# Kernel tuning notes

Hardware: AMD Instinct MI355X
Metric: run time of the kernel (lower is better)

## Reference

```python
import jax, jax.numpy as jnp
import numpy as np

NEG = -9e8

def _leaky(x):
    return jax.nn.leaky_relu(x, 0.01)

def _gru(x, h, wih, whh, bih, bhh):
    # torch.nn.GRUCell math
    gi = x @ wih.T + bih
    gh = h @ whh.T + bhh
    ir, iz, inn = jnp.split(gi, 3, axis=-1)
    hr, hz, hn = jnp.split(gh, 3, axis=-1)
    r = jax.nn.sigmoid(ir + hr)
    z = jax.nn.sigmoid(iz + hz)
    n = jnp.tanh(inn + r * hn)
    return (1.0 - z) * n + z * h

def _gather(feat, idx):
    # feat [B,S,F], idx [B,S,K] -> [B,S,K,F]; -1 wraps to last row, masked later (same as torch)
    return jax.vmap(lambda f, i: f[i])(feat, idx)

def setup_inputs() -> dict:
    key = jax.random.key(0)
    ks = jax.random.split(key, 32)
    B, S, K, F_in, E, R = 32, 512, 21, 26, 256, 3
    amino_list = jax.random.uniform(ks[0], (B, S, F_in), dtype=jnp.float32)
    idx = jax.random.randint(ks[1], (B, S, K), 0, S, dtype=jnp.int32)
    pad = jax.random.uniform(ks[2], (B, S, K)) < 0.3
    amino_degree_list = jnp.where(pad, jnp.int32(-1), idx)
    # variable sequence lengths for mask
    lens = jax.random.randint(ks[3], (B,), S // 2, S + 1)
    amino_mask = (jnp.arange(S)[None, :] < lens[:, None]).astype(jnp.float32)
    s = 0.05
    d = dict(
        amino_list=amino_list,
        amino_degree_list=amino_degree_list,
        amino_mask=amino_mask,
        emb_W=jax.random.normal(ks[4], (E, F_in)) * s,
        emb_b=jax.random.normal(ks[5], (E,)) * s,
        neigh_W=jax.random.normal(ks[6], (E, F_in)) * s,
        neigh_b=jax.random.normal(ks[7], (E,)) * s,
        align_W=jax.random.normal(ks[8], (R, 1, 2 * E)) * s,
        align_b=jax.random.normal(ks[9], (R, 1)) * s,
        attend_W=jax.random.normal(ks[10], (R, E, E)) * s,
        attend_b=jax.random.normal(ks[11], (R, E)) * s,
        gru_wih=jax.random.normal(ks[12], (R, 3 * E, E)) * s,
        gru_whh=jax.random.normal(ks[13], (R, 3 * E, E)) * s,
        gru_bih=jax.random.normal(ks[14], (R, 3 * E)) * s,
        gru_bhh=jax.random.normal(ks[15], (R, 3 * E)) * s,
        seq_align_W=jax.random.normal(ks[16], (1, 2 * E)) * s,
        seq_align_b=jax.random.normal(ks[17], (1,)) * s,
        seq_attend_W=jax.random.normal(ks[18], (E, E)) * s,
        seq_attend_b=jax.random.normal(ks[19], (E,)) * s,
        sgru_wih=jax.random.normal(ks[20], (3 * E, E)) * s,
        sgru_whh=jax.random.normal(ks[21], (3 * E, E)) * s,
        sgru_bih=jax.random.normal(ks[22], (3 * E,)) * s,
        sgru_bhh=jax.random.normal(ks[23], (3 * E,)) * s,
    )
    return d

RADIUS = 3
T_STEPS = 2

def reference(amino_list, amino_degree_list, amino_mask,
              emb_W, emb_b, neigh_W, neigh_b,
              align_W, align_b, attend_W, attend_b,
              gru_wih, gru_whh, gru_bih, gru_bhh,
              seq_align_W, seq_align_b, seq_attend_W, seq_attend_b,
              sgru_wih, sgru_whh, sgru_bih, sgru_bhh):
    B, S, _ = amino_list.shape
    E = emb_W.shape[0]
    K = amino_degree_list.shape[-1]

    mask3 = amino_mask[:, :, None]                       # [B,S,1]
    amino_feature = _leaky(amino_list @ emb_W.T + emb_b)  # [B,S,E]

    attend_mask = (amino_degree_list != -1).astype(jnp.float32)[..., None]   # [B,S,K,1]
    softmax_mask = jnp.where(amino_degree_list == -1, NEG, 0.0)[..., None]   # [B,S,K,1]

    # first radius step: neighbors from raw one-hot features via neighbor_fc
    neighbor = _gather(amino_list, amino_degree_list)                 # [B,S,K,F_in]
    neighbor_feature = _leaky(neighbor @ neigh_W.T + neigh_b)         # [B,S,K,E]

    h = amino_feature.reshape(B * S, E)
    activated = None
    for d in range(RADIUS):
        if d == 0:
            nbr = neighbor_feature
            cur = amino_feature
        else:
            nbr = _gather(activated, amino_degree_list)               # [B,S,K,E]
            cur = activated
        cur_exp = jnp.broadcast_to(cur[:, :, None, :], (B, S, K, E))
        feat_align = jnp.concatenate([cur_exp, nbr], axis=-1)         # [B,S,K,2E]
        score = _leaky(feat_align @ align_W[d].T + align_b[d]) + softmax_mask
        attw = jax.nn.softmax(score, axis=-2) * attend_mask           # [B,S,K,1]
        nbr_t = nbr @ attend_W[d].T + attend_b[d]                     # [B,S,K,E]
        context = jax.nn.elu(jnp.sum(attw * nbr_t, axis=-2))          # [B,S,E]
        h = _gru(context.reshape(B * S, E), h, gru_wih[d], gru_whh[d], gru_bih[d], gru_bhh[d])
        activated = jax.nn.relu(h.reshape(B, S, E))

    seq_feature = jnp.sum(activated * mask3, axis=-2)                 # [B,E]
    act_mol = jax.nn.relu(seq_feature)
    seq_softmax_mask = jnp.where(mask3 == 0.0, NEG, 0.0)              # [B,S,1]

    act_seq = act_mol
    for _ in range(T_STEPS):
        mol_exp = jnp.broadcast_to(act_mol[:, None, :], (B, S, E))
        sa = jnp.concatenate([mol_exp, activated], axis=-1)           # [B,S,2E]
        score = _leaky(sa @ seq_align_W.T + seq_align_b) + seq_softmax_mask
        w = jax.nn.softmax(score, axis=-2) * mask3                    # [B,S,1]
        feat_t = activated @ seq_attend_W.T + seq_attend_b            # [B,S,E]
        seq_context = jax.nn.elu(jnp.sum(w * feat_t, axis=-2))        # [B,E]
        seq_feature = _gru(seq_context, seq_feature, sgru_wih, sgru_whh, sgru_bih, sgru_bhh)
        act_seq = jax.nn.relu(seq_feature)
    return act_seq
```

## Files before the change

kernel.cpp:

```cpp
#include <hip/hip_runtime.h>
#include <hip/hip_bf16.h>
#include <math.h>


#define NEGC (-9.0e8f)

typedef __attribute__((ext_vector_type(8))) short bf16x8;
typedef __attribute__((ext_vector_type(4))) float f32x4;

__device__ __forceinline__ ushort f2bf(float x) {
    union { float f; unsigned u; } v; v.f = x;
    unsigned r = v.u + 0x7FFF + ((v.u >> 16) & 1);
    return (ushort)(r >> 16);
}
__device__ __forceinline__ float bf2f(ushort u) {
    union { unsigned u; float f; } v; v.u = ((unsigned)u) << 16;
    return v.f;
}
__device__ __forceinline__ float sigm_fast(float x) {
    return 1.f / (1.f + __expf(-x));
}
__device__ __forceinline__ float tanh_fast(float x) {
    return 1.f - 2.f / (__expf(2.f * x) + 1.f);
}
__device__ __forceinline__ float elu_fast(float x) {
    return x > 0.f ? x : (__expf(x) - 1.f);
}

typedef const __attribute__((address_space(1))) void gvoid_t;
typedef __attribute__((address_space(3))) void lvoid_t;

__global__ __launch_bounds__(256) void cvt4_kernel(
    const float* __restrict__ s0, ushort* __restrict__ d0, int n0,
    const float* __restrict__ s1, ushort* __restrict__ d1, int n1,
    const float* __restrict__ s2, ushort* __restrict__ d2, int n2,
    const float* __restrict__ s3, ushort* __restrict__ d3, int n3)
{
    int i = blockIdx.x * 256 + threadIdx.x;
    const float* s; ushort* dst; int l;
    if (i < n0) { s = s0; dst = d0; l = i; }
    else if (i < n0 + n1) { s = s1; dst = d1; l = i - n0; }
    else if (i < n0 + n1 + n2) { s = s2; dst = d2; l = i - n0 - n1; }
    else if (i < n0 + n1 + n2 + n3) { s = s3; dst = d3; l = i - n0 - n1 - n2; }
    else return;
    float4 v = *reinterpret_cast<const float4*>(s + (size_t)l * 4);
    ushort4 o; o.x = f2bf(v.x); o.y = f2bf(v.y); o.z = f2bf(v.z); o.w = f2bf(v.w);
    *reinterpret_cast<ushort4*>(dst + (size_t)l * 4) = o;
}

__global__ __launch_bounds__(256) void gemm_dual_kernel(
    const ushort* __restrict__ A0, const ushort* __restrict__ W0,
    const float* __restrict__ b0, ushort* __restrict__ C0, int n0t,
    const ushort* __restrict__ A1, const ushort* __restrict__ W1,
    const float* __restrict__ b1, ushort* __restrict__ C1, int n1t,
    int K,
    const float* __restrict__ dw1, const float* __restrict__ dw2,
    float* __restrict__ dout1, float* __restrict__ dout2)
{
    __shared__ __align__(16) short As[128 * 32];
    __shared__ __align__(16) short Bs[128 * 32];
    int nwg = gridDim.x;
    int q = nwg >> 3;
    int flat = blockIdx.x;
    int sw = (flat & 7) * q + (flat >> 3);
    int tot = n0t + n1t;
    int bmi = sw / tot, bni = sw - bmi * tot;
    const ushort* A; const ushort* W; const float* bias; ushort* C; int N, bn;
    if (bni < n0t) { A = A0; W = W0; bias = b0; C = C0; N = n0t << 7; bn = bni << 7; }
    else { A = A1; W = W1; bias = b1; C = C1; N = n1t << 7; bn = (bni - n0t) << 7; }
    int bm = bmi << 7;

    int tid = threadIdx.x;
    int lane = tid & 63;
    int w = tid >> 6;
    int wr = w >> 1, wc = w & 1;
    bool dots = (dout1 != nullptr) && (bni == 0);

    f32x4 acc[4][4];
#pragma unroll
    for (int m = 0; m < 4; ++m)
#pragma unroll
        for (int n = 0; n < 4; ++n) acc[m][n] = (f32x4){0.f, 0.f, 0.f, 0.f};
    float p1 = 0.f, p2 = 0.f;

    for (int k0 = 0; k0 < K; k0 += 32) {
#pragma unroll
        for (int i = 0; i < 2; ++i) {
            int e = w * 1024 + i * 512 + lane * 8;
            int r = e >> 5, c = e & 31;
            const ushort* ga = A + (size_t)(bm + r) * K + (k0 + c);
            const ushort* gw = W + (size_t)(bn + r) * K + (k0 + c);
            __builtin_amdgcn_global_load_lds((gvoid_t*)ga, (lvoid_t*)&As[w * 1024 + i * 512], 16, 0, 0);
            __builtin_amdgcn_global_load_lds((gvoid_t*)gw, (lvoid_t*)&Bs[w * 1024 + i * 512], 16, 0, 0);
        }
        __syncthreads();
        bf16x8 af[4], bw[4];
        int ra = wr * 64 + (lane & 15);
        int rb = wc * 64 + (lane & 15);
        int kc = (lane >> 4) * 8;
#pragma unroll
        for (int m = 0; m < 4; ++m)
            af[m] = *reinterpret_cast<const bf16x8*>(&As[(ra + m * 16) * 32 + kc]);
#pragma unroll
        for (int n = 0; n < 4; ++n)
            bw[n] = *reinterpret_cast<const bf16x8*>(&Bs[(rb + n * 16) * 32 + kc]);
#pragma unroll
        for (int m = 0; m < 4; ++m)
#pragma unroll
            for (int n = 0; n < 4; ++n)
                acc[m][n] = __builtin_amdgcn_mfma_f32_16x16x32_bf16(af[m], bw[n], acc[m][n], 0, 0, 0);
        if (dots) {
            int drow = tid >> 1, kh = (tid & 1) << 4;
            const short* ar = &As[drow * 32 + kh];
#pragma unroll
            for (int c = 0; c < 16; ++c) {
                float av = bf2f((ushort)ar[c]);
                p1 = fmaf(av, dw1[k0 + kh + c], p1);
                if (dw2) p2 = fmaf(av, dw2[k0 + kh + c], p2);
            }
        }
        __syncthreads();
    }

    if (dots) {
        p1 += __shfl_xor(p1, 1);
        if (dw2) p2 += __shfl_xor(p2, 1);
        if ((tid & 1) == 0) {
            dout1[bm + (tid >> 1)] = p1;
            if (dw2) dout2[bm + (tid >> 1)] = p2;
        }
    }

    int cr0 = bm + wr * 64 + ((lane >> 4) * 4);
    int cc0 = bn + wc * 64 + (lane & 15);
#pragma unroll
    for (int n = 0; n < 4; ++n) {
        int col = cc0 + n * 16;
        float bv = bias[col];
#pragma unroll
        for (int m = 0; m < 4; ++m) {
            int row0 = cr0 + m * 16;
#pragma unroll
            for (int j = 0; j < 4; ++j) {
                float v = acc[m][n][j] + bv;
                C[(size_t)(row0 + j) * N + col] = f2bf(v);
            }
        }
    }
}

__global__ __launch_bounds__(256) void gru_fused_kernel(
    const ushort* __restrict__ ctx, const ushort* __restrict__ wih,
    const float* __restrict__ bih, const ushort* __restrict__ whh,
    const float* __restrict__ bhh,
    const ushort* __restrict__ h_in, ushort* __restrict__ h_out,
    ushort* __restrict__ act_bf)
{
    __shared__ __align__(16) short lds[16384];
    int flat = blockIdx.x;
    int sw = (flat & 7) * 128 + (flat >> 3);
    int bmi = sw >> 2, ct = sw & 3;
    int bm = bmi << 6;
    int tid = threadIdx.x;
    int lane = tid & 63;
    int w = tid >> 6;
    int wr = w >> 1, wc = w & 1;

    f32x4 acc[6][2][2];
#pragma unroll
    for (int qq = 0; qq < 6; ++qq)
#pragma unroll
        for (int m = 0; m < 2; ++m)
#pragma unroll
            for (int n = 0; n < 2; ++n) acc[qq][m][n] = (f32x4){0.f, 0.f, 0.f, 0.f};

    int srow = tid >> 2, scol = (tid & 3) << 3;
    int ldst = (tid & 0xC0) * 8;
    for (int k0 = 0; k0 < 256; k0 += 32) {
        {
            const ushort* s0 = ctx  + (size_t)(bm + srow) * 256 + k0 + scol;
            const ushort* s1 = h_in + (size_t)(bm + srow) * 256 + k0 + scol;
            __builtin_amdgcn_global_load_lds((gvoid_t*)s0, (lvoid_t*)&lds[ldst], 16, 0, 0);
            __builtin_amdgcn_global_load_lds((gvoid_t*)s1, (lvoid_t*)&lds[2048 + ldst], 16, 0, 0);
#pragma unroll
            for (int qq = 0; qq < 6; ++qq) {
                const ushort* wb = (qq < 3) ? wih : whh;
                int slice = (qq < 3) ? qq : qq - 3;
                const ushort* sv = wb + (size_t)(slice * 256 + ct * 64 + srow) * 256 + k0 + scol;
                __builtin_amdgcn_global_load_lds((gvoid_t*)sv,
                    (lvoid_t*)&lds[(2 + qq) * 2048 + ldst], 16, 0, 0);
            }
        }
        __syncthreads();
        int rl = lane & 15;
        int kc = (lane >> 4) * 8;
        bf16x8 a_c[2], a_h[2];
#pragma unroll
        for (int m = 0; m < 2; ++m) {
            a_c[m] = *reinterpret_cast<const bf16x8*>(&lds[(wr * 32 + m * 16 + rl) * 32 + kc]);
            a_h[m] = *reinterpret_cast<const bf16x8*>(&lds[2048 + (wr * 32 + m * 16 + rl) * 32 + kc]);
        }
#pragma unroll
        for (int qq = 0; qq < 6; ++qq) {
            bf16x8 bw[2];
#pragma unroll
            for (int n = 0; n < 2; ++n)
                bw[n] = *reinterpret_cast<const bf16x8*>(
                    &lds[(2 + qq) * 2048 + (wc * 32 + n * 16 + rl) * 32 + kc]);
#pragma unroll
            for (int m = 0; m < 2; ++m)
#pragma unroll
                for (int n = 0; n < 2; ++n)
                    acc[qq][m][n] = __builtin_amdgcn_mfma_f32_16x16x32_bf16(
                        (qq < 3) ? a_c[m] : a_h[m], bw[n], acc[qq][m][n], 0, 0, 0);
        }
        __syncthreads();
    }

#pragma unroll
    for (int n = 0; n < 2; ++n) {
        int col = ct * 64 + wc * 32 + n * 16 + (lane & 15);
        float bir = bih[col], biz = bih[256 + col], bin = bih[512 + col];
        float bhr = bhh[col], bhz = bhh[256 + col], bhn = bhh[512 + col];
#pragma unroll
        for (int m = 0; m < 2; ++m) {
            int row0 = bm + wr * 32 + m * 16 + ((lane >> 4) * 4);
#pragma unroll
            for (int j = 0; j < 4; ++j) {
                size_t idx = (size_t)(row0 + j) * 256 + col;
                float r = sigm_fast(acc[0][m][n][j] + bir + acc[3][m][n][j] + bhr);
                float z = sigm_fast(acc[1][m][n][j] + biz + acc[4][m][n][j] + bhz);
                float nn = tanh_fast(acc[2][m][n][j] + bin + r * (acc[5][m][n][j] + bhn));
                float hold = bf2f(h_in[idx]);
                float hh = (1.f - z) * nn + z * hold;
                h_out[idx] = f2bf(hh);
                act_bf[idx] = f2bf(fmaxf(hh, 0.f));
            }
        }
    }
}

__global__ __launch_bounds__(256) void embed_kernel(
    const float* __restrict__ amino, const float* __restrict__ embW,
    const float* __restrict__ embB, const float* __restrict__ neighW,
    const float* __restrict__ neighB,
    ushort* __restrict__ h_bf, ushort* __restrict__ nf_bf)
{
    const int FIN = 26, FPAD = 28, ROWS = 64;
    __shared__ __align__(16) float xs[ROWS][FPAD];
    int tid = threadIdx.x;
    float wE[FPAD], wN[FPAD];
#pragma unroll
    for (int f = 0; f < FIN; ++f) {
        wE[f] = embW[tid * FIN + f];
        wN[f] = neighW[tid * FIN + f];
    }
    wE[26] = wE[27] = wN[26] = wN[27] = 0.f;
    float b1 = embB[tid], b2 = neighB[tid];
    int row0 = blockIdx.x * ROWS;
    for (int idx = tid; idx < ROWS * FPAD; idx += 256) {
        int r = idx / FPAD, f = idx - r * FPAD;
        xs[r][f] = (f < FIN) ? amino[(size_t)(row0 + r) * FIN + f] : 0.f;
    }
    __syncthreads();
    for (int r = 0; r < ROWS; ++r) {
        const float4* x4 = reinterpret_cast<const float4*>(xs[r]);
        float a = b1, c = b2;
#pragma unroll
        for (int q = 0; q < 7; ++q) {
            float4 x = x4[q];
            a = fmaf(x.x, wE[4 * q], a);     c = fmaf(x.x, wN[4 * q], c);
            a = fmaf(x.y, wE[4 * q + 1], a); c = fmaf(x.y, wN[4 * q + 1], c);
            a = fmaf(x.z, wE[4 * q + 2], a); c = fmaf(x.z, wN[4 * q + 2], c);
            a = fmaf(x.w, wE[4 * q + 3], a); c = fmaf(x.w, wN[4 * q + 3], c);
        }
        a = a > 0.f ? a : 0.01f * a;
        c = c > 0.f ? c : 0.01f * c;
        size_t idx = (size_t)(row0 + r) * 256 + tid;
        h_bf[idx] = f2bf(a);
        nf_bf[idx] = f2bf(c);
    }
}

__global__ __launch_bounds__(256) void rowdots_bf16_kernel(
    const ushort* __restrict__ cur, const ushort* __restrict__ nbr,
    const float* __restrict__ alignW, float* __restrict__ ca, float* __restrict__ cb)
{
    int tid = threadIdx.x;
    int wv = tid >> 6, lane = tid & 63;
    size_t row = (size_t)blockIdx.x * 4 + wv;
    int e0 = lane * 4;
    ushort4 cv = *reinterpret_cast<const ushort4*>(cur + row * 256 + e0);
    ushort4 nv = *reinterpret_cast<const ushort4*>(nbr + row * 256 + e0);
    float4 w1 = *reinterpret_cast<const float4*>(alignW + e0);
    float4 w2 = *reinterpret_cast<const float4*>(alignW + 256 + e0);
    float p1 = bf2f(cv.x) * w1.x + bf2f(cv.y) * w1.y + bf2f(cv.z) * w1.z + bf2f(cv.w) * w1.w;
    float p2 = bf2f(nv.x) * w2.x + bf2f(nv.y) * w2.y + bf2f(nv.z) * w2.z + bf2f(nv.w) * w2.w;
#pragma unroll
    for (int off = 32; off > 0; off >>= 1) {
        p1 += __shfl_down(p1, off);
        p2 += __shfl_down(p2, off);
    }
    if (lane == 0) { ca[row] = p1; cb[row] = p2; }
}

__global__ __launch_bounds__(256) void attn_kernel(
    const int* __restrict__ deg, const float* __restrict__ ca,
    const float* __restrict__ cbrow, const ushort* __restrict__ act_t,
    const float* __restrict__ alignB, int d,
    ushort* __restrict__ context_bf, int S)
{
    const int KNB = 21;
    int raw = blockIdx.x;
    int bid = (raw & 7) * 512 + (raw >> 3);
    int bs0 = bid * 4;
    int b = bs0 >> 9;
    int tid = threadIdx.x;
    int wv = tid >> 6, lane = tid & 63;
    int bs = bs0 + wv;
    __shared__ float ss[4][KNB];
    __shared__ int   sj[4][KNB];
    if (lane < KNB) {
        int j = deg[bs * KNB + lane];
        float cbv = (j >= 0) ? cbrow[b * S + j] : 0.f;
        float sc = ca[bs] + cbv + alignB[d];
        sc = sc > 0.f ? sc : 0.01f * sc;
        if (j < 0) sc += NEGC;
        sj[wv][lane] = j;
        ss[wv][lane] = sc;
    }
    __syncthreads();
    float mx = -3.4e38f;
#pragma unroll
    for (int k = 0; k < KNB; ++k) mx = fmaxf(mx, ss[wv][k]);
    float se[KNB];
    float sum = 0.f;
#pragma unroll
    for (int k = 0; k < KNB; ++k) { se[k] = __expf(ss[wv][k] - mx); sum += se[k]; }
    float inv = 1.f / sum;
    const ushort* base = act_t + (size_t)b * S * 256 + lane * 4;
    float a0 = 0.f, a1 = 0.f, a2 = 0.f, a3 = 0.f;
#pragma unroll
    for (int k = 0; k < KNB; ++k) {
        int j = sj[wv][k];
        if (j >= 0) {
            ushort4 v = *reinterpret_cast<const ushort4*>(base + (size_t)j * 256);
            float wk = se[k];
            a0 = fmaf(wk, bf2f(v.x), a0);
            a1 = fmaf(wk, bf2f(v.y), a1);
            a2 = fmaf(wk, bf2f(v.z), a2);
            a3 = fmaf(wk, bf2f(v.w), a3);
        }
    }
    ushort4 o;
    o.x = f2bf(elu_fast(a0 * inv));
    o.y = f2bf(elu_fast(a1 * inv));
    o.z = f2bf(elu_fast(a2 * inv));
    o.w = f2bf(elu_fast(a3 * inv));
    *reinterpret_cast<ushort4*>(&context_bf[(size_t)bs * 256 + lane * 4]) = o;
}

__global__ __launch_bounds__(256) void seqpool_partial_kernel(
    const ushort* __restrict__ act, const float* __restrict__ mask,
    float* __restrict__ partial, int S, int CH)
{
    int bc = blockIdx.x;
    int NC = S / CH;
    int b = bc / NC, c = bc - b * NC;
    int tid = threadIdx.x;
    int s0 = c * CH;
    const ushort* ab = act + ((size_t)b * S + s0) * 256;
    const float* mb = mask + b * S + s0;
    float acc = 0.f;
    for (int s = 0; s < CH; ++s)
        acc = fmaf(bf2f(ab[(size_t)s * 256 + tid]), mb[s], acc);
    partial[(size_t)bc * 256 + tid] = acc;
}

__global__ __launch_bounds__(256) void seqpool_sm_kernel(
    const float* __restrict__ partial, const float* __restrict__ saW,
    const float* __restrict__ praw, const float* __restrict__ sab,
    const float* __restrict__ mask,
    float* __restrict__ seqfeat, float* __restrict__ wout, int NC, int S)
{
    int b = blockIdx.x, tid = threadIdx.x;
    int lane = tid & 63, wv = tid >> 6;
    __shared__ float red[4];
    __shared__ float sw[512];
    __shared__ float r1[4], r2[4];
    __shared__ float smd;
    float acc = 0.f;
    for (int c = 0; c < NC; ++c)
        acc += partial[((size_t)b * NC + c) * 256 + tid];
    seqfeat[b * 256 + tid] = acc;
    float am = fmaxf(acc, 0.f);
    float p = am * saW[tid];
#pragma unroll
    for (int off = 32; off > 0; off >>= 1) p += __shfl_down(p, off);
    if (lane == 0) red[wv] = p;
    __syncthreads();
    if (tid == 0) smd = red[0] + red[1] + red[2] + red[3];
    __syncthreads();
    float md = smd, sb = sab[0];
    float lm = -3.4e38f;
    for (int s = tid; s < S; s += 256) {
        float sc = md + praw[b * S + s] + sb;
        sc = sc > 0.f ? sc : 0.01f * sc;
        if (mask[b * S + s] == 0.f) sc += NEGC;
        sw[s] = sc;
        lm = fmaxf(lm, sc);
    }
#pragma unroll
    for (int off = 32; off > 0; off >>= 1) lm = fmaxf(lm, __shfl_down(lm, off));
    if (lane == 0) r1[wv] = lm;
    __syncthreads();
    float mx = fmaxf(fmaxf(r1[0], r1[1]), fmaxf(r1[2], r1[3]));
    float ls = 0.f;
    for (int s = tid; s < S; s += 256) {
        float e = __expf(sw[s] - mx);
        sw[s] = e * mask[b * S + s];
        ls += e;
    }
#pragma unroll
    for (int off = 32; off > 0; off >>= 1) ls += __shfl_down(ls, off);
    if (lane == 0) r2[wv] = ls;
    __syncthreads();
    float inv = 1.f / (r2[0] + r2[1] + r2[2] + r2[3]);
    for (int s = tid; s < S; s += 256)
        wout[b * S + s] = sw[s] * inv;
}

__global__ __launch_bounds__(256) void seqctx_partial_kernel(
    const float* __restrict__ w, const ushort* __restrict__ feat,
    float* __restrict__ partial, int S, int CH)
{
    int bc = blockIdx.x;
    int NC = S / CH;
    int b = bc / NC, c = bc - b * NC;
    int tid = threadIdx.x;
    int s0 = c * CH;
    const ushort* fb = feat + ((size_t)b * S + s0) * 256;
    const float* wb = w + b * S + s0;
    float acc = 0.f;
    for (int s = 0; s < CH; ++s)
        acc = fmaf(wb[s], bf2f(fb[(size_t)s * 256 + tid]), acc);
    partial[(size_t)bc * 256 + tid] = acc;
}

__global__ __launch_bounds__(256) void seqctx_combine_kernel(
    const float* __restrict__ partial, float* __restrict__ sctx, int NC)
{
    int b = blockIdx.x, tid = threadIdx.x;
    float acc = 0.f;
    for (int c = 0; c < NC; ++c)
        acc += partial[((size_t)b * NC + c) * 256 + tid];
    sctx[b * 256 + tid] = elu_fast(acc);
}

__global__ __launch_bounds__(256) void sgru_mm_kernel(
    const float* __restrict__ x, const float* __restrict__ hseq,
    const float* __restrict__ wih, const float* __restrict__ whh,
    const float* __restrict__ bih, const float* __restrict__ bhh,
    float* __restrict__ g, int full)
{
    int per_b = full ? 1536 : 768;
    int o = blockIdx.x * 4 + (threadIdx.x >> 6);
    int lane = threadIdx.x & 63;
    int b = o / per_b;
    int j = o - b * per_b;
    if (!full) j += 768;
    const float* src; const float* w; const float* bp; int jj;
    if (j < 768) { src = x + b * 256; w = wih; bp = bih; jj = j; }
    else         { src = hseq + b * 256; w = whh; bp = bhh; jj = j - 768; }
    float p = 0.f;
#pragma unroll
    for (int i = 0; i < 4; ++i) {
        int idx = lane + 64 * i;
        p = fmaf(src[idx], w[(size_t)jj * 256 + idx], p);
    }
#pragma unroll
    for (int off = 32; off > 0; off >>= 1) p += __shfl_down(p, off);
    if (lane == 0) g[b * 1536 + j] = p + bp[jj];
}

__global__ __launch_bounds__(256) void sgru_gate_kernel(
    const float* __restrict__ g, float* __restrict__ hseq, float* __restrict__ out)
{
    int b = blockIdx.x, e = threadIdx.x;
    const float* gr = g + b * 1536;
    float r = sigm_fast(gr[e] + gr[768 + e]);
    float z = sigm_fast(gr[256 + e] + gr[1024 + e]);
    float n = tanh_fast(gr[512 + e] + r * gr[1280 + e]);
    float hv = hseq[b * 256 + e];
    float hn = (1.f - z) * n + z * hv;
    hseq[b * 256 + e] = hn;
    out[b * 256 + e] = fmaxf(hn, 0.f);
}

extern "C" void kernel_launch(void* const* d_in, const int* in_sizes, int n_in,
                              void* d_out, int out_size, void* d_ws, size_t ws_size,
                              hipStream_t stream)
{
    const float* amino   = (const float*)d_in[0];
    const int*   deg     = (const int*)  d_in[1];
    const float* mask    = (const float*)d_in[2];
    const float* embW    = (const float*)d_in[3];
    const float* embB    = (const float*)d_in[4];
    const float* neighW  = (const float*)d_in[5];
    const float* neighB  = (const float*)d_in[6];
    const float* alignW  = (const float*)d_in[7];
    const float* alignB  = (const float*)d_in[8];
    const float* attendW = (const float*)d_in[9];
    const float* attendB = (const float*)d_in[10];
    const float* gruWih  = (const float*)d_in[11];
    const float* gruWhh  = (const float*)d_in[12];
    const float* gruBih  = (const float*)d_in[13];
    const float* gruBhh  = (const float*)d_in[14];
    const float* saW     = (const float*)d_in[15];
    const float* saB     = (const float*)d_in[16];
    const float* seqAttW = (const float*)d_in[17];
    const float* seqAttB = (const float*)d_in[18];
    const float* sWih    = (const float*)d_in[19];
    const float* sWhh    = (const float*)d_in[20];
    const float* sBih    = (const float*)d_in[21];
    const float* sBhh    = (const float*)d_in[22];
    float* out = (float*)d_out;

    const int B = 32, S = 512;
    const int BS = B * S;
    const size_t N1 = (size_t)BS * 256;
    const int CH = 32, NC = S / CH;

    ushort* hA     = (ushort*)d_ws;
    ushort* hB     = hA + N1;
    ushort* act_bf = hB + N1;
    ushort* nb_bf  = act_bf + N1;
    ushort* att_bf = nb_bf + N1;
    ushort* attW_bf = att_bf + N1;
    ushort* wih_bf  = attW_bf + 3 * 256 * 256;
    ushort* whh_bf  = wih_bf + 3 * 768 * 256;
    ushort* saW2_bf = whh_bf + 3 * 768 * 256;
    float* smalls = (float*)(saW2_bf + 256 * 256);
    float* ca   = smalls;
    float* cb   = ca + BS;
    float* scor = cb + BS;
    float* wbuf = scor + BS;
    float* seqf = wbuf + BS;
    float* sctx = seqf + B * 256;
    float* g    = sctx + B * 256;
    float* part = g + B * 1536;

    const int c0 = (3 * 256 * 256) / 4, c1 = (3 * 768 * 256) / 4,
              c2 = (3 * 768 * 256) / 4, c3 = (256 * 256) / 4;
    cvt4_kernel<<<(c0 + c1 + c2 + c3 + 255) / 256, 256, 0, stream>>>(
        attendW, attW_bf, c0, gruWih, wih_bf, c1, gruWhh, whh_bf, c2, seqAttW, saW2_bf, c3);

    embed_kernel<<<BS / 64, 256, 0, stream>>>(amino, embW, embB, neighW, neighB,
                                              hA, nb_bf);
    rowdots_bf16_kernel<<<BS / 4, 256, 0, stream>>>(hA, nb_bf, alignW, ca, cb);

    for (int d = 0; d < 3; ++d) {
        const ushort* nbr_bf = (d == 0) ? nb_bf : act_bf;
        const ushort* h_in  = (d & 1) ? hB : hA;
        ushort*       h_out = (d & 1) ? hA : hB;
        gemm_dual_kernel<<<128 * 2, 256, 0, stream>>>(
            nbr_bf, attW_bf + d * 256 * 256, attendB + d * 256, att_bf, 2,
            (const ushort*)nullptr, (const ushort*)nullptr, (const float*)nullptr,
            (ushort*)nullptr, 0, 256,
            d == 0 ? (const float*)nullptr : alignW + d * 512,
            d == 0 ? (const float*)nullptr : alignW + d * 512 + 256,
            d == 0 ? (float*)nullptr : ca,
            d == 0 ? (float*)nullptr : cb);
        attn_kernel<<<BS / 4, 256, 0, stream>>>(deg, ca, cb, att_bf, alignB, d, nb_bf, S);
        gru_fused_kernel<<<1024, 256, 0, stream>>>(
            nb_bf, wih_bf + d * 768 * 256, gruBih + d * 768,
            whh_bf + d * 768 * 256, gruBhh + d * 768, h_in, h_out, act_bf);
    }

    seqpool_partial_kernel<<<B * NC, 256, 0, stream>>>(act_bf, mask, part, S, CH);
    gemm_dual_kernel<<<128 * 2, 256, 0, stream>>>(
        act_bf, saW2_bf, seqAttB, att_bf, 2,
        (const ushort*)nullptr, (const ushort*)nullptr, (const float*)nullptr,
        (ushort*)nullptr, 0, 256,
        saW + 256, (const float*)nullptr, scor, (float*)nullptr);
    seqpool_sm_kernel<<<B, 256, 0, stream>>>(part, saW, scor, saB, mask, seqf, wbuf, NC, S);
    seqctx_partial_kernel<<<B * NC, 256, 0, stream>>>(wbuf, att_bf, part, S, CH);
    seqctx_combine_kernel<<<B, 256, 0, stream>>>(part, sctx, NC);

    sgru_mm_kernel<<<B * 1536 / 4, 256, 0, stream>>>(sctx, seqf, sWih, sWhh, sBih, sBhh, g, 1);
    sgru_gate_kernel<<<B, 256, 0, stream>>>(g, seqf, out);
    sgru_mm_kernel<<<B * 768 / 4, 256, 0, stream>>>(sctx, seqf, sWih, sWhh, sBih, sBhh, g, 0);
    sgru_gate_kernel<<<B, 256, 0, stream>>>(g, seqf, out);
}
```

Baseline: 287.3 us.

## Aggregate neighbors before attend GEMM and fuse it into GRU kernel

Uses linearity to swap the order of operations: the softmax-weighted neighbor sum is now taken over raw features first (u), and the attend projection is applied afterwards as a 32-row GEMM inside the GRU kernel, with the bias scaled by the sum of weights. This removes the full per-layer attend GEMM and its intermediate buffer. The next layer's align row-dots are accumulated with atomics, and the final layer's masked sequence pooling is computed in the GRU epilogue, replacing separate kernels. In exchange the GRU kernel carries extra per-block weight loads and needs memsets for the atomic accumulators. Tiles shrink to 32 rows, so the grid doubles.

```diff
diff --git a/kernel.cpp b/kernel.cpp
--- a/kernel.cpp
+++ b/kernel.cpp
@@ -150,92 +150,189 @@
 }
 
 __global__ __launch_bounds__(256) void gru_fused_kernel(
-    const ushort* __restrict__ ctx, const ushort* __restrict__ wih,
-    const float* __restrict__ bih, const ushort* __restrict__ whh,
-    const float* __restrict__ bhh,
+    const ushort* __restrict__ u, const float* __restrict__ swsum,
+    const ushort* __restrict__ Wa, const float* __restrict__ ba,
+    const ushort* __restrict__ wih, const float* __restrict__ bih,
+    const ushort* __restrict__ whh, const float* __restrict__ bhh,
     const ushort* __restrict__ h_in, ushort* __restrict__ h_out,
-    ushort* __restrict__ act_bf)
-{
-    __shared__ __align__(16) short lds[16384];
+    ushort* __restrict__ act_bf,
+    const float* __restrict__ dw1, const float* __restrict__ dw2,
+    float* __restrict__ dca, float* __restrict__ dcb,
+    const float* __restrict__ mask, float* __restrict__ pool_part)
+{
+    __shared__ __align__(16) short lds[21760];
+    const int CTX = 13312;
     int flat = blockIdx.x;
-    int sw = (flat & 7) * 128 + (flat >> 3);
+    int sw = (flat & 7) * 256 + (flat >> 3);
     int bmi = sw >> 2, ct = sw & 3;
-    int bm = bmi << 6;
+    int bm = bmi << 5;
     int tid = threadIdx.x;
     int lane = tid & 63;
     int w = tid >> 6;
+    int rl = lane & 15;
+    int kc = (lane >> 4) * 8;
+    int r0 = (lane >> 4) * 4;
+
+    f32x4 accA[2][4];
+#pragma unroll
+    for (int m = 0; m < 2; ++m)
+#pragma unroll
+        for (int n = 0; n < 4; ++n) accA[m][n] = (f32x4){0.f, 0.f, 0.f, 0.f};
+
+    for (int k0 = 0; k0 < 256; k0 += 32) {
+        for (int ch = w; ch < 18; ch += 4) {
+            const ushort* g;
+            if (ch < 2) {
+                int e = ch * 512 + lane * 8;
+                g = u + (size_t)(bm + (e >> 5)) * 256 + k0 + (e & 31);
+            } else {
+                int e = (ch - 2) * 512 + lane * 8;
+                g = Wa + (size_t)(e >> 5) * 256 + k0 + (e & 31);
+            }
+            __builtin_amdgcn_global_load_lds((gvoid_t*)g, (lvoid_t*)&lds[ch * 512], 16, 0, 0);
+        }
+        __syncthreads();
+        bf16x8 au0 = *reinterpret_cast<const bf16x8*>(&lds[rl * 32 + kc]);
+        bf16x8 au1 = *reinterpret_cast<const bf16x8*>(&lds[(16 + rl) * 32 + kc]);
+#pragma unroll
+        for (int n = 0; n < 4; ++n) {
+            bf16x8 bW = *reinterpret_cast<const bf16x8*>(
+                &lds[1024 + (w * 64 + n * 16 + rl) * 32 + kc]);
+            accA[0][n] = __builtin_amdgcn_mfma_f32_16x16x32_bf16(au0, bW, accA[0][n], 0, 0, 0);
+            accA[1][n] = __builtin_amdgcn_mfma_f32_16x16x32_bf16(au1, bW, accA[1][n], 0, 0, 0);
+        }
+        __syncthreads();
+    }
+
+    {
+        float swv[2][4];
+#pragma unroll
+        for (int m = 0; m < 2; ++m)
+#pragma unroll
+            for (int j = 0; j < 4; ++j)
+                swv[m][j] = swsum[bm + m * 16 + r0 + j];
+#pragma unroll
+        for (int n = 0; n < 4; ++n) {
+            int col = w * 64 + n * 16 + rl;
+            float bav = ba[col];
+#pragma unroll
+            for (int m = 0; m < 2; ++m)
+#pragma unroll
+                for (int j = 0; j < 4; ++j) {
+                    float v = elu_fast(accA[m][n][j] + swv[m][j] * bav);
+                    lds[CTX + (m * 16 + r0 + j) * 264 + col] = (short)f2bf(v);
+                }
+        }
+    }
+    __syncthreads();
+
     int wr = w >> 1, wc = w & 1;
-
-    f32x4 acc[6][2][2];
+    f32x4 accB[6][2];
 #pragma unroll
     for (int qq = 0; qq < 6; ++qq)
 #pragma unroll
-        for (int m = 0; m < 2; ++m)
-#pragma unroll
-            for (int n = 0; n < 2; ++n) acc[qq][m][n] = (f32x4){0.f, 0.f, 0.f, 0.f};
-
-    int srow = tid >> 2, scol = (tid & 3) << 3;
-    int ldst = (tid & 0xC0) * 8;
+        for (int n = 0; n < 2; ++n) accB[qq][n] = (f32x4){0.f, 0.f, 0.f, 0.f};
+
     for (int k0 = 0; k0 < 256; k0 += 32) {
-        {
-            const ushort* s0 = ctx  + (size_t)(bm + srow) * 256 + k0 + scol;
-            const ushort* s1 = h_in + (size_t)(bm + srow) * 256 + k0 + scol;
-            __builtin_amdgcn_global_load_lds((gvoid_t*)s0, (lvoid_t*)&lds[ldst], 16, 0, 0);
-            __builtin_amdgcn_global_load_lds((gvoid_t*)s1, (lvoid_t*)&lds[2048 + ldst], 16, 0, 0);
-#pragma unroll
-            for (int qq = 0; qq < 6; ++qq) {
+        for (int ch = w; ch < 26; ch += 4) {
+            const ushort* g;
+            if (ch < 2) {
+                int e = ch * 512 + lane * 8;
+                g = h_in + (size_t)(bm + (e >> 5)) * 256 + k0 + (e & 31);
+            } else {
+                int idx = ch - 2;
+                int qq = idx >> 2;
+                int e = (idx & 3) * 512 + lane * 8;
                 const ushort* wb = (qq < 3) ? wih : whh;
-                int slice = (qq < 3) ? qq : qq - 3;
-                const ushort* sv = wb + (size_t)(slice * 256 + ct * 64 + srow) * 256 + k0 + scol;
-                __builtin_amdgcn_global_load_lds((gvoid_t*)sv,
-                    (lvoid_t*)&lds[(2 + qq) * 2048 + ldst], 16, 0, 0);
+                int sl = (qq < 3) ? qq : qq - 3;
+                g = wb + (size_t)(sl * 256 + ct * 64 + (e >> 5)) * 256 + k0 + (e & 31);
             }
+            __builtin_amdgcn_global_load_lds((gvoid_t*)g, (lvoid_t*)&lds[ch * 512], 16, 0, 0);
         }
         __syncthreads();
-        int rl = lane & 15;
-        int kc = (lane >> 4) * 8;
-        bf16x8 a_c[2], a_h[2];
-#pragma unroll
-        for (int m = 0; m < 2; ++m) {
-            a_c[m] = *reinterpret_cast<const bf16x8*>(&lds[(wr * 32 + m * 16 + rl) * 32 + kc]);
-            a_h[m] = *reinterpret_cast<const bf16x8*>(&lds[2048 + (wr * 32 + m * 16 + rl) * 32 + kc]);
-        }
+        bf16x8 a_c = *reinterpret_cast<const bf16x8*>(&lds[CTX + (wr * 16 + rl) * 264 + k0 + kc]);
+        bf16x8 a_h = *reinterpret_cast<const bf16x8*>(&lds[(wr * 16 + rl) * 32 + kc]);
 #pragma unroll
         for (int qq = 0; qq < 6; ++qq) {
-            bf16x8 bw[2];
-#pragma unroll
-            for (int n = 0; n < 2; ++n)
-                bw[n] = *reinterpret_cast<const bf16x8*>(
-                    &lds[(2 + qq) * 2048 + (wc * 32 + n * 16 + rl) * 32 + kc]);
-#pragma unroll
-            for (int m = 0; m < 2; ++m)
-#pragma unroll
-                for (int n = 0; n < 2; ++n)
-                    acc[qq][m][n] = __builtin_amdgcn_mfma_f32_16x16x32_bf16(
-                        (qq < 3) ? a_c[m] : a_h[m], bw[n], acc[qq][m][n], 0, 0, 0);
+#pragma unroll
+            for (int n = 0; n < 2; ++n) {
+                bf16x8 bw = *reinterpret_cast<const bf16x8*>(
+                    &lds[1024 + qq * 2048 + (wc * 32 + n * 16 + rl) * 32 + kc]);
+                accB[qq][n] = __builtin_amdgcn_mfma_f32_16x16x32_bf16(
+                    (qq < 3) ? a_c : a_h, bw, accB[qq][n], 0, 0, 0);
+            }
         }
         __syncthreads();
     }
 
+    float actv[2][4];
 #pragma unroll
     for (int n = 0; n < 2; ++n) {
-        int col = ct * 64 + wc * 32 + n * 16 + (lane & 15);
+        int col = ct * 64 + wc * 32 + n * 16 + rl;
         float bir = bih[col], biz = bih[256 + col], bin = bih[512 + col];
         float bhr = bhh[col], bhz = bhh[256 + col], bhn = bhh[512 + col];
 #pragma unroll
-        for (int m = 0; m < 2; ++m) {
-            int row0 = bm + wr * 32 + m * 16 + ((lane >> 4) * 4);
-#pragma unroll
-            for (int j = 0; j < 4; ++j) {
-                size_t idx = (size_t)(row0 + j) * 256 + col;
-                float r = sigm_fast(acc[0][m][n][j] + bir + acc[3][m][n][j] + bhr);
-                float z = sigm_fast(acc[1][m][n][j] + biz + acc[4][m][n][j] + bhz);
-                float nn = tanh_fast(acc[2][m][n][j] + bin + r * (acc[5][m][n][j] + bhn));
-                float hold = bf2f(h_in[idx]);
-                float hh = (1.f - z) * nn + z * hold;
-                h_out[idx] = f2bf(hh);
-                act_bf[idx] = f2bf(fmaxf(hh, 0.f));
+        for (int j = 0; j < 4; ++j) {
+            int row = bm + wr * 16 + r0 + j;
+            size_t idx = (size_t)row * 256 + col;
+            float r = sigm_fast(accB[0][n][j] + bir + accB[3][n][j] + bhr);
+            float z = sigm_fast(accB[1][n][j] + biz + accB[4][n][j] + bhz);
+            float nn = tanh_fast(accB[2][n][j] + bin + r * (accB[5][n][j] + bhn));
+            float hold = bf2f(h_in[idx]);
+            float hh = (1.f - z) * nn + z * hold;
+            h_out[idx] = f2bf(hh);
+            float a = fmaxf(hh, 0.f);
+            act_bf[idx] = f2bf(a);
+            actv[n][j] = a;
+        }
+    }
+
+    if (dca) {
+        float w1v[2], w2v[2];
+#pragma unroll
+        for (int n = 0; n < 2; ++n) {
+            int col = ct * 64 + wc * 32 + n * 16 + rl;
+            w1v[n] = dw1[col];
+            w2v[n] = dw2[col];
+        }
+#pragma unroll
+        for (int j = 0; j < 4; ++j) {
+            float p1 = actv[0][j] * w1v[0] + actv[1][j] * w1v[1];
+            float p2 = actv[0][j] * w2v[0] + actv[1][j] * w2v[1];
+#pragma unroll
+            for (int mk = 1; mk < 16; mk <<= 1) {
+                p1 += __shfl_xor(p1, mk);
+                p2 += __shfl_xor(p2, mk);
             }
+            if (rl == 0) {
+                int row = bm + wr * 16 + r0 + j;
+                atomicAdd(&dca[row], p1);
+                atomicAdd(&dcb[row], p2);
+            }
+        }
+    }
+
+    if (pool_part) {
+        float* buf = (float*)lds;
+        int b_ = bm >> 9;
+        int sbase = bm & 511;
+        float pm0 = 0.f, pm1 = 0.f;
+#pragma unroll
+        for (int j = 0; j < 4; ++j) {
+            int sr = wr * 16 + r0 + j;
+            float mv = mask[b_ * 512 + sbase + sr];
+            pm0 = fmaf(actv[0][j], mv, pm0);
+            pm1 = fmaf(actv[1][j], mv, pm1);
+        }
+        int contrib = wr * 4 + (lane >> 4);
+        buf[contrib * 64 + wc * 32 + rl] = pm0;
+        buf[contrib * 64 + wc * 32 + 16 + rl] = pm1;
+        __syncthreads();
+        if (tid < 64) {
+            float s2 = 0.f;
+#pragma unroll
+            for (int i = 0; i < 8; ++i) s2 += buf[i * 64 + tid];
+            pool_part[((size_t)b_ * 16 + (sbase >> 5)) * 256 + ct * 64 + tid] = s2;
         }
     }
 }
@@ -304,11 +401,11 @@
     if (lane == 0) { ca[row] = p1; cb[row] = p2; }
 }
 
-__global__ __launch_bounds__(256) void attn_kernel(
+__global__ __launch_bounds__(256) void attn_u_kernel(
     const int* __restrict__ deg, const float* __restrict__ ca,
-    const float* __restrict__ cbrow, const ushort* __restrict__ act_t,
+    const float* __restrict__ cbrow, const ushort* __restrict__ src,
     const float* __restrict__ alignB, int d,
-    ushort* __restrict__ context_bf, int S)
+    ushort* __restrict__ u_bf, float* __restrict__ swsum, int S)
 {
     const int KNB = 21;
     int raw = blockIdx.x;
@@ -338,14 +435,16 @@
 #pragma unroll
     for (int k = 0; k < KNB; ++k) { se[k] = __expf(ss[wv][k] - mx); sum += se[k]; }
     float inv = 1.f / sum;
-    const ushort* base = act_t + (size_t)b * S * 256 + lane * 4;
+    const ushort* base = src + (size_t)b * S * 256 + lane * 4;
     float a0 = 0.f, a1 = 0.f, a2 = 0.f, a3 = 0.f;
+    float sumv = 0.f;
 #pragma unroll
     for (int k = 0; k < KNB; ++k) {
         int j = sj[wv][k];
         if (j >= 0) {
             ushort4 v = *reinterpret_cast<const ushort4*>(base + (size_t)j * 256);
             float wk = se[k];
+            sumv += wk;
             a0 = fmaf(wk, bf2f(v.x), a0);
             a1 = fmaf(wk, bf2f(v.y), a1);
             a2 = fmaf(wk, bf2f(v.z), a2);
@@ -353,28 +452,12 @@
         }
     }
     ushort4 o;
-    o.x = f2bf(elu_fast(a0 * inv));
-    o.y = f2bf(elu_fast(a1 * inv));
-    o.z = f2bf(elu_fast(a2 * inv));
-    o.w = f2bf(elu_fast(a3 * inv));
-    *reinterpret_cast<ushort4*>(&context_bf[(size_t)bs * 256 + lane * 4]) = o;
-}
-
-__global__ __launch_bounds__(256) void seqpool_partial_kernel(
-    const ushort* __restrict__ act, const float* __restrict__ mask,
-    float* __restrict__ partial, int S, int CH)
-{
-    int bc = blockIdx.x;
-    int NC = S / CH;
-    int b = bc / NC, c = bc - b * NC;
-    int tid = threadIdx.x;
-    int s0 = c * CH;
-    const ushort* ab = act + ((size_t)b * S + s0) * 256;
-    const float* mb = mask + b * S + s0;
-    float acc = 0.f;
-    for (int s = 0; s < CH; ++s)
-        acc = fmaf(bf2f(ab[(size_t)s * 256 + tid]), mb[s], acc);
-    partial[(size_t)bc * 256 + tid] = acc;
+    o.x = f2bf(a0 * inv);
+    o.y = f2bf(a1 * inv);
+    o.z = f2bf(a2 * inv);
+    o.w = f2bf(a3 * inv);
+    *reinterpret_cast<ushort4*>(&u_bf[(size_t)bs * 256 + lane * 4]) = o;
+    if (lane == 0) swsum[bs] = sumv * inv;
 }
 
 __global__ __launch_bounds__(256) void seqpool_sm_kernel(
@@ -529,26 +612,26 @@
     const int B = 32, S = 512;
     const int BS = B * S;
     const size_t N1 = (size_t)BS * 256;
-    const int CH = 32, NC = S / CH;
 
     ushort* hA     = (ushort*)d_ws;
     ushort* hB     = hA + N1;
     ushort* act_bf = hB + N1;
     ushort* nb_bf  = act_bf + N1;
-    ushort* att_bf = nb_bf + N1;
-    ushort* attW_bf = att_bf + N1;
+    ushort* u_bf   = nb_bf + N1;
+    ushort* attW_bf = u_bf + N1;
     ushort* wih_bf  = attW_bf + 3 * 256 * 256;
     ushort* whh_bf  = wih_bf + 3 * 768 * 256;
     ushort* saW2_bf = whh_bf + 3 * 768 * 256;
     float* smalls = (float*)(saW2_bf + 256 * 256);
-    float* ca   = smalls;
-    float* cb   = ca + BS;
-    float* scor = cb + BS;
-    float* wbuf = scor + BS;
-    float* seqf = wbuf + BS;
-    float* sctx = seqf + B * 256;
-    float* g    = sctx + B * 256;
-    float* part = g + B * 1536;
+    float* ca    = smalls;
+    float* cb    = ca + BS;
+    float* scor  = cb + BS;
+    float* wbuf  = scor + BS;
+    float* swsum = wbuf + BS;
+    float* seqf  = swsum + BS;
+    float* sctx  = seqf + B * 256;
+    float* g     = sctx + B * 256;
+    float* part  = g + B * 1536;
 
     const int c0 = (3 * 256 * 256) / 4, c1 = (3 * 768 * 256) / 4,
               c2 = (3 * 768 * 256) / 4, c3 = (256 * 256) / 4;
@@ -560,32 +643,34 @@
     rowdots_bf16_kernel<<<BS / 4, 256, 0, stream>>>(hA, nb_bf, alignW, ca, cb);
 
     for (int d = 0; d < 3; ++d) {
-        const ushort* nbr_bf = (d == 0) ? nb_bf : act_bf;
+        const ushort* gsrc = (d == 0) ? nb_bf : act_bf;
         const ushort* h_in  = (d & 1) ? hB : hA;
         ushort*       h_out = (d & 1) ? hA : hB;
-        gemm_dual_kernel<<<128 * 2, 256, 0, stream>>>(
-            nbr_bf, attW_bf + d * 256 * 256, attendB + d * 256, att_bf, 2,
-            (const ushort*)nullptr, (const ushort*)nullptr, (const float*)nullptr,
-            (ushort*)nullptr, 0, 256,
-            d == 0 ? (const float*)nullptr : alignW + d * 512,
-            d == 0 ? (const float*)nullptr : alignW + d * 512 + 256,
-            d == 0 ? (float*)nullptr : ca,
-            d == 0 ? (float*)nullptr : cb);
-        attn_kernel<<<BS / 4, 256, 0, stream>>>(deg, ca, cb, att_bf, alignB, d, nb_bf, S);
-        gru_fused_kernel<<<1024, 256, 0, stream>>>(
-            nb_bf, wih_bf + d * 768 * 256, gruBih + d * 768,
-            whh_bf + d * 768 * 256, gruBhh + d * 768, h_in, h_out, act_bf);
-    }
-
-    seqpool_partial_kernel<<<B * NC, 256, 0, stream>>>(act_bf, mask, part, S, CH);
+        attn_u_kernel<<<BS / 4, 256, 0, stream>>>(deg, ca, cb, gsrc, alignB, d,
+                                                  u_bf, swsum, S);
+        if (d < 2)
+            hipMemsetAsync(ca, 0, (size_t)2 * BS * sizeof(float), stream);
+        gru_fused_kernel<<<2048, 256, 0, stream>>>(
+            u_bf, swsum, attW_bf + d * 256 * 256, attendB + d * 256,
+            wih_bf + d * 768 * 256, gruBih + d * 768,
+            whh_bf + d * 768 * 256, gruBhh + d * 768,
+            h_in, h_out, act_bf,
+            (d < 2) ? alignW + (d + 1) * 512 : (const float*)nullptr,
+            (d < 2) ? alignW + (d + 1) * 512 + 256 : (const float*)nullptr,
+            (d < 2) ? ca : (float*)nullptr,
+            (d < 2) ? cb : (float*)nullptr,
+            (d == 2) ? mask : (const float*)nullptr,
+            (d == 2) ? part : (float*)nullptr);
+    }
+
     gemm_dual_kernel<<<128 * 2, 256, 0, stream>>>(
-        act_bf, saW2_bf, seqAttB, att_bf, 2,
+        act_bf, saW2_bf, seqAttB, u_bf, 2,
         (const ushort*)nullptr, (const ushort*)nullptr, (const float*)nullptr,
         (ushort*)nullptr, 0, 256,
         saW + 256, (const float*)nullptr, scor, (float*)nullptr);
-    seqpool_sm_kernel<<<B, 256, 0, stream>>>(part, saW, scor, saB, mask, seqf, wbuf, NC, S);
-    seqctx_partial_kernel<<<B * NC, 256, 0, stream>>>(wbuf, att_bf, part, S, CH);
-    seqctx_combine_kernel<<<B, 256, 0, stream>>>(part, sctx, NC);
+    seqpool_sm_kernel<<<B, 256, 0, stream>>>(part, saW, scor, saB, mask, seqf, wbuf, 16, S);
+    seqctx_partial_kernel<<<B * 16, 256, 0, stream>>>(wbuf, u_bf, part, S, 32);
+    seqctx_combine_kernel<<<B, 256, 0, stream>>>(part, sctx, 16);
 
     sgru_mm_kernel<<<B * 1536 / 4, 256, 0, stream>>>(sctx, seqf, sWih, sWhh, sBih, sBhh, g, 1);
     sgru_gate_kernel<<<B, 256, 0, stream>>>(g, seqf, out);
```

Result: slower. 349.0 us (+21.5%).

## Fuse align row-dots into embed and masked seq-pool into last GRU

Applied to the files above, without the earlier changes.

The standalone rowdots kernel goes away. Its two align dot products are now computed inside embed_kernel through wave shuffles and an LDS reduction across the four waves. The seqpool_partial kernel is also removed: the final-depth GRU epilogue accumulates the masked relu activations per 32-row chunk and writes the partials directly. This saves two launches and two full re-reads of the BS×256 bf16 activations, at the cost of extra reduction work and a barrier in embed plus slightly more register use in the GRU epilogue.

```diff
diff --git a/kernel.cpp b/kernel.cpp
--- a/kernel.cpp
+++ b/kernel.cpp
@@ -154,7 +154,8 @@
     const float* __restrict__ bih, const ushort* __restrict__ whh,
     const float* __restrict__ bhh,
     const ushort* __restrict__ h_in, ushort* __restrict__ h_out,
-    ushort* __restrict__ act_bf)
+    ushort* __restrict__ act_bf,
+    const float* __restrict__ mask, float* __restrict__ pool_part)
 {
     __shared__ __align__(16) short lds[16384];
     int flat = blockIdx.x;
@@ -217,14 +218,28 @@
         __syncthreads();
     }
 
+    int rl = lane & 15;
+    int r0 = (lane >> 4) * 4;
+    float mv[2][4];
+    if (pool_part) {
+        int b_ = bm >> 9;
+        int sbase = bm & 511;
+#pragma unroll
+        for (int m = 0; m < 2; ++m)
+#pragma unroll
+            for (int j = 0; j < 4; ++j)
+                mv[m][j] = mask[b_ * 512 + sbase + wr * 32 + m * 16 + r0 + j];
+    }
+    float pm[2] = {0.f, 0.f};
+
 #pragma unroll
     for (int n = 0; n < 2; ++n) {
-        int col = ct * 64 + wc * 32 + n * 16 + (lane & 15);
+        int col = ct * 64 + wc * 32 + n * 16 + rl;
         float bir = bih[col], biz = bih[256 + col], bin = bih[512 + col];
         float bhr = bhh[col], bhz = bhh[256 + col], bhn = bhh[512 + col];
 #pragma unroll
         for (int m = 0; m < 2; ++m) {
-            int row0 = bm + wr * 32 + m * 16 + ((lane >> 4) * 4);
+            int row0 = bm + wr * 32 + m * 16 + r0;
 #pragma unroll
             for (int j = 0; j < 4; ++j) {
                 size_t idx = (size_t)(row0 + j) * 256 + col;
@@ -234,7 +249,24 @@
                 float hold = bf2f(h_in[idx]);
                 float hh = (1.f - z) * nn + z * hold;
                 h_out[idx] = f2bf(hh);
-                act_bf[idx] = f2bf(fmaxf(hh, 0.f));
+                float a = fmaxf(hh, 0.f);
+                act_bf[idx] = f2bf(a);
+                if (pool_part) pm[n] = fmaf(a, mv[m][j], pm[n]);
+            }
+        }
+    }
+
+    if (pool_part) {
+#pragma unroll
+        for (int n = 0; n < 2; ++n) {
+            float p = pm[n];
+            p += __shfl_xor(p, 16);
+            p += __shfl_xor(p, 32);
+            if (lane < 16) {
+                int b_ = bm >> 9;
+                int sc = ((bm & 511) >> 5) + wr;
+                int col = ct * 64 + wc * 32 + n * 16 + rl;
+                pool_part[((size_t)b_ * 16 + sc) * 256 + col] = p;
             }
         }
     }
@@ -243,12 +275,16 @@
 __global__ __launch_bounds__(256) void embed_kernel(
     const float* __restrict__ amino, const float* __restrict__ embW,
     const float* __restrict__ embB, const float* __restrict__ neighW,
-    const float* __restrict__ neighB,
-    ushort* __restrict__ h_bf, ushort* __restrict__ nf_bf)
+    const float* __restrict__ neighB, const float* __restrict__ alignW,
+    ushort* __restrict__ h_bf, ushort* __restrict__ nf_bf,
+    float* __restrict__ ca, float* __restrict__ cb)
 {
     const int FIN = 26, FPAD = 28, ROWS = 64;
     __shared__ __align__(16) float xs[ROWS][FPAD];
+    __shared__ float red1[ROWS][4];
+    __shared__ float red2[ROWS][4];
     int tid = threadIdx.x;
+    int lane = tid & 63, wv = tid >> 6;
     float wE[FPAD], wN[FPAD];
 #pragma unroll
     for (int f = 0; f < FIN; ++f) {
@@ -257,6 +293,7 @@
     }
     wE[26] = wE[27] = wN[26] = wN[27] = 0.f;
     float b1 = embB[tid], b2 = neighB[tid];
+    float w1t = alignW[tid], w2t = alignW[256 + tid];
     int row0 = blockIdx.x * ROWS;
     for (int idx = tid; idx < ROWS * FPAD; idx += 256) {
         int r = idx / FPAD, f = idx - r * FPAD;
@@ -279,29 +316,21 @@
         size_t idx = (size_t)(row0 + r) * 256 + tid;
         h_bf[idx] = f2bf(a);
         nf_bf[idx] = f2bf(c);
-    }
-}
-
-__global__ __launch_bounds__(256) void rowdots_bf16_kernel(
-    const ushort* __restrict__ cur, const ushort* __restrict__ nbr,
-    const float* __restrict__ alignW, float* __restrict__ ca, float* __restrict__ cb)
-{
-    int tid = threadIdx.x;
-    int wv = tid >> 6, lane = tid & 63;
-    size_t row = (size_t)blockIdx.x * 4 + wv;
-    int e0 = lane * 4;
-    ushort4 cv = *reinterpret_cast<const ushort4*>(cur + row * 256 + e0);
-    ushort4 nv = *reinterpret_cast<const ushort4*>(nbr + row * 256 + e0);
-    float4 w1 = *reinterpret_cast<const float4*>(alignW + e0);
-    float4 w2 = *reinterpret_cast<const float4*>(alignW + 256 + e0);
-    float p1 = bf2f(cv.x) * w1.x + bf2f(cv.y) * w1.y + bf2f(cv.z) * w1.z + bf2f(cv.w) * w1.w;
-    float p2 = bf2f(nv.x) * w2.x + bf2f(nv.y) * w2.y + bf2f(nv.z) * w2.z + bf2f(nv.w) * w2.w;
-#pragma unroll
-    for (int off = 32; off > 0; off >>= 1) {
-        p1 += __shfl_down(p1, off);
-        p2 += __shfl_down(p2, off);
-    }
-    if (lane == 0) { ca[row] = p1; cb[row] = p2; }
+        float p1 = a * w1t, p2 = c * w2t;
+#pragma unroll
+        for (int off = 32; off > 0; off >>= 1) {
+            p1 += __shfl_down(p1, off);
+            p2 += __shfl_down(p2, off);
+        }
+        if (lane == 0) { red1[r][wv] = p1; red2[r][wv] = p2; }
+    }
+    __syncthreads();
+    if (tid < ROWS)
+        ca[row0 + tid] = red1[tid][0] + red1[tid][1] + red1[tid][2] + red1[tid][3];
+    else if (tid < 2 * ROWS) {
+        int r = tid - ROWS;
+        cb[row0 + r] = red2[r][0] + red2[r][1] + red2[r][2] + red2[r][3];
+    }
 }
 
 __global__ __launch_bounds__(256) void attn_kernel(
@@ -358,23 +387,6 @@
     o.z = f2bf(elu_fast(a2 * inv));
     o.w = f2bf(elu_fast(a3 * inv));
     *reinterpret_cast<ushort4*>(&context_bf[(size_t)bs * 256 + lane * 4]) = o;
-}
-
-__global__ __launch_bounds__(256) void seqpool_partial_kernel(
-    const ushort* __restrict__ act, const float* __restrict__ mask,
-    float* __restrict__ partial, int S, int CH)
-{
-    int bc = blockIdx.x;
-    int NC = S / CH;
-    int b = bc / NC, c = bc - b * NC;
-    int tid = threadIdx.x;
-    int s0 = c * CH;
-    const ushort* ab = act + ((size_t)b * S + s0) * 256;
-    const float* mb = mask + b * S + s0;
-    float acc = 0.f;
-    for (int s = 0; s < CH; ++s)
-        acc = fmaf(bf2f(ab[(size_t)s * 256 + tid]), mb[s], acc);
-    partial[(size_t)bc * 256 + tid] = acc;
 }
 
 __global__ __launch_bounds__(256) void seqpool_sm_kernel(
@@ -529,7 +541,6 @@
     const int B = 32, S = 512;
     const int BS = B * S;
     const size_t N1 = (size_t)BS * 256;
-    const int CH = 32, NC = S / CH;
 
     ushort* hA     = (ushort*)d_ws;
     ushort* hB     = hA + N1;
@@ -555,9 +566,8 @@
     cvt4_kernel<<<(c0 + c1 + c2 + c3 + 255) / 256, 256, 0, stream>>>(
         attendW, attW_bf, c0, gruWih, wih_bf, c1, gruWhh, whh_bf, c2, seqAttW, saW2_bf, c3);
 
-    embed_kernel<<<BS / 64, 256, 0, stream>>>(amino, embW, embB, neighW, neighB,
-                                              hA, nb_bf);
-    rowdots_bf16_kernel<<<BS / 4, 256, 0, stream>>>(hA, nb_bf, alignW, ca, cb);
+    embed_kernel<<<BS / 64, 256, 0, stream>>>(amino, embW, embB, neighW, neighB, alignW,
+                                              hA, nb_bf, ca, cb);
 
     for (int d = 0; d < 3; ++d) {
         const ushort* nbr_bf = (d == 0) ? nb_bf : act_bf;
@@ -574,18 +584,19 @@
         attn_kernel<<<BS / 4, 256, 0, stream>>>(deg, ca, cb, att_bf, alignB, d, nb_bf, S);
         gru_fused_kernel<<<1024, 256, 0, stream>>>(
             nb_bf, wih_bf + d * 768 * 256, gruBih + d * 768,
-            whh_bf + d * 768 * 256, gruBhh + d * 768, h_in, h_out, act_bf);
-    }
-
-    seqpool_partial_kernel<<<B * NC, 256, 0, stream>>>(act_bf, mask, part, S, CH);
+            whh_bf + d * 768 * 256, gruBhh + d * 768, h_in, h_out, act_bf,
+            (d == 2) ? mask : (const float*)nullptr,
+            (d == 2) ? part : (float*)nullptr);
+    }
+
     gemm_dual_kernel<<<128 * 2, 256, 0, stream>>>(
         act_bf, saW2_bf, seqAttB, att_bf, 2,
         (const ushort*)nullptr, (const ushort*)nullptr, (const float*)nullptr,
         (ushort*)nullptr, 0, 256,
         saW + 256, (const float*)nullptr, scor, (float*)nullptr);
-    seqpool_sm_kernel<<<B, 256, 0, stream>>>(part, saW, scor, saB, mask, seqf, wbuf, NC, S);
-    seqctx_partial_kernel<<<B * NC, 256, 0, stream>>>(wbuf, att_bf, part, S, CH);
-    seqctx_combine_kernel<<<B, 256, 0, stream>>>(part, sctx, NC);
+    seqpool_sm_kernel<<<B, 256, 0, stream>>>(part, saW, scor, saB, mask, seqf, wbuf, 16, S);
+    seqctx_partial_kernel<<<B * 16, 256, 0, stream>>>(wbuf, att_bf, part, S, 32);
+    seqctx_combine_kernel<<<B, 256, 0, stream>>>(part, sctx, 16);
 
     sgru_mm_kernel<<<B * 1536 / 4, 256, 0, stream>>>(sctx, seqf, sWih, sWhh, sBih, sBhh, g, 1);
     sgru_gate_kernel<<<B, 256, 0, stream>>>(g, seqf, out);
```

Measured after the change: 284.3 us. Within noise of the previous version (-1.0%).
